# Performance work log

Measured on AMD Instinct MI355X. Metric: run time of the kernel, lower is better.

## Reference

```python
import jax, jax.numpy as jnp
import numpy as np

N, D, H, C = 50000, 256, 4, 16  # nodes, in_dim, heads, out_channels (hidden_dim)
E = 1600000
NEG_SLOPE = 0.2


def _gatv2_layer(x, src, dst, Wl, bl, Wr, br, att, bias, n_nodes):
    """PyG GATv2Conv (share_weights=False, concat=True, eval mode).
    x: [N, Fin]; Wl/Wr: [Fin, H*C]; att: [H, C]; bias: [H*C].
    """
    xl = (x @ Wl + bl).reshape(n_nodes, H, C)  # source-side transform
    xr = (x @ Wr + br).reshape(n_nodes, H, C)  # target-side transform
    # per-edge attention logits: a^T LeakyReLU(xl_j + xr_i)
    e = jax.nn.leaky_relu(xl[src] + xr[dst], negative_slope=NEG_SLOPE)  # [E,H,C]
    logits = jnp.einsum('ehc,hc->eh', e, att)  # [E,H]
    # scatter-softmax over incoming edges of each target node
    m = jax.ops.segment_max(logits, dst, num_segments=n_nodes)  # [N,H]
    ex = jnp.exp(logits - m[dst])
    denom = jax.ops.segment_sum(ex, dst, num_segments=n_nodes)  # [N,H]
    alpha = ex / denom[dst]  # [E,H]
    out = jax.ops.segment_sum(alpha[:, :, None] * xl[src], dst, num_segments=n_nodes)
    return out.reshape(n_nodes, H * C) + bias


def setup_inputs() -> dict:
    key = jax.random.key(0)
    ks = jax.random.split(key, 16)
    g = lambda k, shp, fan: jax.random.normal(k, shp, jnp.float32) * (1.0 / np.sqrt(fan))
    inp = {
        'x': jax.random.normal(ks[0], (N, D), jnp.float32),
        'edge_index': jax.random.randint(ks[1], (2, E), 0, N, dtype=jnp.int64),
        # conv1: in D -> H*C
        'Wl1': g(ks[2], (D, H * C), D), 'bl1': jnp.zeros((H * C,), jnp.float32),
        'Wr1': g(ks[3], (D, H * C), D), 'br1': jnp.zeros((H * C,), jnp.float32),
        'att1': g(ks[4], (H, C), C), 'bias1': jnp.zeros((H * C,), jnp.float32),
        # conv2: in H*C -> H*C
        'Wl2': g(ks[5], (H * C, H * C), H * C), 'bl2': jnp.zeros((H * C,), jnp.float32),
        'Wr2': g(ks[6], (H * C, H * C), H * C), 'br2': jnp.zeros((H * C,), jnp.float32),
        'att2': g(ks[7], (H, C), C), 'bias2': jnp.zeros((H * C,), jnp.float32),
        # output head: H*C -> D
        'Wo': g(ks[8], (H * C, D), H * C), 'bo': jnp.zeros((D,), jnp.float32),
    }
    return inp


def reference(x, edge_index, Wl1, bl1, Wr1, br1, att1, bias1,
              Wl2, bl2, Wr2, br2, att2, bias2, Wo, bo):
    src, dst = edge_index[0], edge_index[1]
    h = jax.nn.relu(_gatv2_layer(x, src, dst, Wl1, bl1, Wr1, br1, att1, bias1, N))
    h = jax.nn.relu(_gatv2_layer(h, src, dst, Wl2, bl2, Wr2, br2, att2, bias2, N))
    return jax.nn.sigmoid(h @ Wo + bo)  # min_max is None -> no affine rescale
```

## Files before the change

kernel.cpp:

```cpp
#include <hip/hip_runtime.h>
#include <math.h>

#define NN 50000
#define DIN 256
#define HC 64
#define NEG 0.2f
#define TM 64
#define NB 196
#define EPB 4096
#define CAP 36864

typedef short bf16x8 __attribute__((ext_vector_type(8)));
typedef unsigned short ush8 __attribute__((ext_vector_type(8)));
typedef float f32x4 __attribute__((ext_vector_type(4)));

__device__ __forceinline__ unsigned short f2bf(float x) {
    unsigned u = __float_as_uint(x);
    u += 0x7FFFu + ((u >> 16) & 1u);
    return (unsigned short)(u >> 16);
}
__device__ __forceinline__ float bf2f(unsigned short h) {
    return __uint_as_float((unsigned)h << 16);
}

template <int CTRL>
__device__ __forceinline__ float dpp_mov(float x) {
    int r = __builtin_amdgcn_update_dpp(0, __float_as_int(x), CTRL, 0xF, 0xF, true);
    return __int_as_float(r);
}


__global__ __launch_bounds__(256) void bhist_k(const int* __restrict__ dst,
                                               int* __restrict__ bcnt, int E) {
    __shared__ int h[NB];
    int t = threadIdx.x;
    for (int i = t; i < NB; i += 256) h[i] = 0;
    __syncthreads();
    int base = blockIdx.x * 2048 + t;
#pragma unroll
    for (int k = 0; k < 8; ++k) {
        int e = base + k * 256;
        if (e < E) atomicAdd(&h[dst[e] >> 8], 1);
    }
    __syncthreads();
    for (int i = t; i < NB; i += 256)
        if (h[i]) atomicAdd(&bcnt[i], h[i]);
}

__global__ __launch_bounds__(256) void bscan_k(const int* __restrict__ bcnt,
                                               int* __restrict__ boffs,
                                               int* __restrict__ bcursor,
                                               int* __restrict__ offs, int E) {
    __shared__ int s[256];
    int t = threadIdx.x;
    s[t] = (t < NB) ? bcnt[t] : 0;
    __syncthreads();
    for (int off = 1; off < 256; off <<= 1) {
        int v = s[t];
        int u = (t >= off) ? s[t - off] : 0;
        __syncthreads();
        s[t] = v + u;
        __syncthreads();
    }
    if (t < NB) {
        int ex = (t == 0) ? 0 : s[t - 1];
        boffs[t] = ex;
        bcursor[t] = ex;
    }
    if (t == NB) boffs[NB] = s[NB - 1];
    if (t == 0) offs[NN] = E;
}

__global__ __launch_bounds__(1024) void bin_k(const int* __restrict__ src,
                                              const int* __restrict__ dst,
                                              int* __restrict__ bcursor,
                                              unsigned* __restrict__ epair, int E) {
    __shared__ int hist[NB];
    __shared__ int lofs[NB];
    __shared__ int gshift[NB];
    __shared__ int scanb[256];
    __shared__ unsigned pbuf[EPB];
    __shared__ unsigned char abkt[EPB];
    int t = threadIdx.x;
    for (int i = t; i < NB; i += 1024) hist[i] = 0;
    __syncthreads();
    int e0 = blockIdx.x * EPB;
    unsigned p[4]; int bk[4], rk[4]; bool val[4];
#pragma unroll
    for (int k = 0; k < 4; ++k) {
        int e = e0 + k * 1024 + t;
        val[k] = e < E;
        if (val[k]) {
            int s = src[e], d = dst[e];
            p[k] = ((unsigned)s << 8) | (unsigned)(d & 255);
            bk[k] = d >> 8;
            rk[k] = atomicAdd(&hist[bk[k]], 1);
        }
    }
    __syncthreads();
    if (t < 256) scanb[t] = (t < NB) ? hist[t] : 0;
    __syncthreads();
    for (int off = 1; off < 256; off <<= 1) {
        int v = 0, u = 0;
        if (t < 256) { v = scanb[t]; if (t >= off) u = scanb[t - off]; }
        __syncthreads();
        if (t < 256) scanb[t] = v + u;
        __syncthreads();
    }
    if (t < NB) {
        int ex = (t == 0) ? 0 : scanb[t - 1];
        lofs[t] = ex;
        int gb = atomicAdd(&bcursor[t], hist[t]);
        gshift[t] = gb - ex;
    }
    __syncthreads();
    int total = scanb[NB - 1];
#pragma unroll
    for (int k = 0; k < 4; ++k) {
        if (val[k]) {
            int pos = lofs[bk[k]] + rk[k];
            pbuf[pos] = p[k];
            abkt[pos] = (unsigned char)bk[k];
        }
    }
    __syncthreads();
    for (int i = t; i < total; i += 1024) {
        int b = abkt[i];
        epair[gshift[b] + i] = pbuf[i];
    }
}

__global__ __launch_bounds__(1024) void bsort_k(const unsigned* __restrict__ epair,
                                                const int* __restrict__ boffs,
                                                int* __restrict__ offs,
                                                unsigned* __restrict__ ssrc, int n) {
    __shared__ int lhist[256];
    __shared__ int lcur[256];
    __shared__ int scanb[256];
    __shared__ unsigned sbuf[CAP];
    int b = blockIdx.x, t = threadIdx.x;
    int start = boffs[b], end = boffs[b + 1];
    int cnt = end - start;
    if (t < 256) lhist[t] = 0;
    __syncthreads();
    for (int i = t; i < cnt; i += 1024) {
        unsigned p = epair[start + i];
        atomicAdd(&lhist[p & 255], 1);
    }
    __syncthreads();
    if (t < 256) scanb[t] = lhist[t];
    __syncthreads();
    for (int off = 1; off < 256; off <<= 1) {
        int v = 0, u = 0;
        if (t < 256) { v = scanb[t]; if (t >= off) u = scanb[t - off]; }
        __syncthreads();
        if (t < 256) scanb[t] = v + u;
        __syncthreads();
    }
    if (t < 256) {
        int ex = (t == 0) ? 0 : scanb[t - 1];
        lcur[t] = ex;
        int node = b * 256 + t;
        if (node < n) offs[node] = start + ex;
    }
    __syncthreads();
    if (cnt <= CAP) {
        for (int i = t; i < cnt; i += 1024) {
            unsigned p = epair[start + i];
            int r = atomicAdd(&lcur[p & 255], 1);
            sbuf[r] = p & ~255u;
        }
        __syncthreads();
        for (int i = t; i < cnt; i += 1024) ssrc[start + i] = sbuf[i] >> 1;
    } else {
        for (int i = t; i < cnt; i += 1024) {
            unsigned p = epair[start + i];
            int r = atomicAdd(&lcur[p & 255], 1);
            ssrc[start + r] = (p & ~255u) >> 1;
        }
    }
}

__global__ __launch_bounds__(256) void wprep_dual_k(const float* __restrict__ Wl,
                                                    const float* __restrict__ Wr,
                                                    unsigned short* __restrict__ img,
                                                    int K) {
    int i = blockIdx.x * 256 + threadIdx.x;
    int total = (K >> 5) * 10240;
    if (i >= total) return;
    int kk = i % 40;
    int c  = (i / 40) & 127;
    int p  = (i / 5120) & 1;
    int s  = i / 10240;
    unsigned short v = 0;
    if (kk < 32) {
        int k = s * 32 + kk;
        float w = (c < 64) ? Wl[k * HC + c] : Wr[k * HC + (c - 64)];
        unsigned short hi = f2bf(w);
        v = p ? f2bf(w - bf2f(hi)) : hi;
    }
    img[i] = v;
}

__global__ __launch_bounds__(256) void wprep_head_k(const float* __restrict__ Wo,
                                                    unsigned short* __restrict__ img) {
    int i = blockIdx.x * 256 + threadIdx.x;
    if (i >= 40960) return;
    int kk = i % 40;
    int c  = (i / 40) & 127;
    int p  = (i / 5120) & 1;
    int s  = (i / 10240) & 1;
    int h  = i / 20480;
    unsigned short v = 0;
    if (kk < 32) {
        int k = s * 32 + kk;
        float w = Wo[k * DIN + h * 128 + c];
        unsigned short hi = f2bf(w);
        v = p ? f2bf(w - bf2f(hi)) : hi;
    }
    img[i] = v;
}

__global__ __launch_bounds__(256) void gemm_dual_mfma_k(
        const float* __restrict__ A,
        const unsigned short* __restrict__ img,
        const float* __restrict__ bl, const float* __restrict__ br,
        _Float16* __restrict__ xlh, float* __restrict__ xr,
        int n, int K) {
    __shared__ __attribute__((aligned(16))) unsigned short As[2][64][40];
    __shared__ __attribute__((aligned(16))) unsigned short Bs[2][128][40];
    int t = threadIdx.x;
    int l = t & 63, w = t >> 6;
    int wr = w >> 1, wc = w & 1;
    int lan = l & 15;
    int kb  = (l >> 4) * 8;
    int row0 = blockIdx.x * 64;
    int srow = t >> 2;
    int skq  = (t & 3) * 8;
    bool rok = (row0 + srow) < n;
    const float* aptr = A + (size_t)(row0 + srow) * K + skq;

    f32x4 acc0[4] = {}, acc1[4] = {};

    int nks = K >> 5;
    for (int ks = 0; ks < nks; ++ks) {
        __syncthreads();
        {
            const ush8* src = (const ush8*)(img + (size_t)ks * 10240);
            ush8* dst = (ush8*)&Bs[0][0][0];
            int base = w * 5 * 64 + l;
#pragma unroll
            for (int c2 = 0; c2 < 5; ++c2) {
                int u = base + c2 * 64;
                dst[u] = src[u];
            }
        }
        {
            float4 f0 = make_float4(0.f, 0.f, 0.f, 0.f), f1 = f0;
            if (rok) {
                f0 = *(const float4*)(aptr + ks * 32);
                f1 = *(const float4*)(aptr + ks * 32 + 4);
            }
            float xs[8] = {f0.x, f0.y, f0.z, f0.w, f1.x, f1.y, f1.z, f1.w};
            ush8 hi8, lo8;
#pragma unroll
            for (int j = 0; j < 8; ++j) {
                unsigned short h = f2bf(xs[j]);
                hi8[j] = h;
                lo8[j] = f2bf(xs[j] - bf2f(h));
            }
            *(ush8*)&As[0][srow][skq] = hi8;
            *(ush8*)&As[1][srow][skq] = lo8;
        }
        __syncthreads();
        bf16x8 ah0 = *(const bf16x8*)&As[0][wr * 32 + lan][kb];
        bf16x8 ah1 = *(const bf16x8*)&As[0][wr * 32 + 16 + lan][kb];
        bf16x8 al0 = *(const bf16x8*)&As[1][wr * 32 + lan][kb];
        bf16x8 al1 = *(const bf16x8*)&As[1][wr * 32 + 16 + lan][kb];
#pragma unroll
        for (int cf = 0; cf < 4; ++cf) {
            int bc = wc * 64 + cf * 16 + lan;
            bf16x8 bhv = *(const bf16x8*)&Bs[0][bc][kb];
            bf16x8 blv = *(const bf16x8*)&Bs[1][bc][kb];
            acc0[cf] = __builtin_amdgcn_mfma_f32_16x16x32_bf16(ah0, bhv, acc0[cf], 0, 0, 0);
            acc1[cf] = __builtin_amdgcn_mfma_f32_16x16x32_bf16(ah1, bhv, acc1[cf], 0, 0, 0);
            acc0[cf] = __builtin_amdgcn_mfma_f32_16x16x32_bf16(al0, bhv, acc0[cf], 0, 0, 0);
            acc1[cf] = __builtin_amdgcn_mfma_f32_16x16x32_bf16(al1, bhv, acc1[cf], 0, 0, 0);
            acc0[cf] = __builtin_amdgcn_mfma_f32_16x16x32_bf16(ah0, blv, acc0[cf], 0, 0, 0);
            acc1[cf] = __builtin_amdgcn_mfma_f32_16x16x32_bf16(ah1, blv, acc1[cf], 0, 0, 0);
        }
    }
#pragma unroll
    for (int cf = 0; cf < 4; ++cf) {
        int col = wc * 64 + cf * 16 + lan;
        bool left = col < 64;
        float bv = left ? bl[col] : br[col - 64];
        int c2 = left ? col : col - 64;
#pragma unroll
        for (int rf = 0; rf < 2; ++rf) {
            f32x4 a = rf ? acc1[cf] : acc0[cf];
            int rbase = row0 + wr * 32 + rf * 16 + (l >> 4) * 4;
#pragma unroll
            for (int r = 0; r < 4; ++r) {
                int grow = rbase + r;
                if (grow < n) {
                    float v = a[r] + bv;
                    if (left) xlh[(size_t)grow * HC + c2] = (_Float16)v;
                    else      xr[(size_t)grow * HC + c2] = v;
                }
            }
        }
    }
}

__global__ __launch_bounds__(256) void head_gemm_mfma_k(
        const float* __restrict__ A,
        const unsigned short* __restrict__ img,
        const float* __restrict__ bo,
        float* __restrict__ out, int n) {
    __shared__ __attribute__((aligned(16))) unsigned short As[2][64][40];
    __shared__ __attribute__((aligned(16))) unsigned short Bs[2][128][40];
    int t = threadIdx.x;
    int l = t & 63, w = t >> 6;
    int wr = w >> 1, wc = w & 1;
    int lan = l & 15;
    int kb  = (l >> 4) * 8;
    int row0 = blockIdx.x * 64;
    int coloff = blockIdx.y * 128;
    const unsigned short* himg = img + (size_t)blockIdx.y * 2 * 10240;
    int srow = t >> 2;
    int skq  = (t & 3) * 8;
    bool rok = (row0 + srow) < n;
    const float* aptr = A + (size_t)(row0 + srow) * HC + skq;

    f32x4 acc0[4] = {}, acc1[4] = {};

    for (int ks = 0; ks < 2; ++ks) {
        __syncthreads();
        {
            const ush8* src = (const ush8*)(himg + (size_t)ks * 10240);
            ush8* dst = (ush8*)&Bs[0][0][0];
            int base = w * 5 * 64 + l;
#pragma unroll
            for (int c2 = 0; c2 < 5; ++c2) {
                int u = base + c2 * 64;
                dst[u] = src[u];
            }
        }
        {
            float4 f0 = make_float4(0.f, 0.f, 0.f, 0.f), f1 = f0;
            if (rok) {
                f0 = *(const float4*)(aptr + ks * 32);
                f1 = *(const float4*)(aptr + ks * 32 + 4);
            }
            float xs[8] = {f0.x, f0.y, f0.z, f0.w, f1.x, f1.y, f1.z, f1.w};
            ush8 hi8, lo8;
#pragma unroll
            for (int j = 0; j < 8; ++j) {
                unsigned short h = f2bf(xs[j]);
                hi8[j] = h;
                lo8[j] = f2bf(xs[j] - bf2f(h));
            }
            *(ush8*)&As[0][srow][skq] = hi8;
            *(ush8*)&As[1][srow][skq] = lo8;
        }
        __syncthreads();
        bf16x8 ah0 = *(const bf16x8*)&As[0][wr * 32 + lan][kb];
        bf16x8 ah1 = *(const bf16x8*)&As[0][wr * 32 + 16 + lan][kb];
        bf16x8 al0 = *(const bf16x8*)&As[1][wr * 32 + lan][kb];
        bf16x8 al1 = *(const bf16x8*)&As[1][wr * 32 + 16 + lan][kb];
#pragma unroll
        for (int cf = 0; cf < 4; ++cf) {
            int bc = wc * 64 + cf * 16 + lan;
            bf16x8 bhv = *(const bf16x8*)&Bs[0][bc][kb];
            bf16x8 blv = *(const bf16x8*)&Bs[1][bc][kb];
            acc0[cf] = __builtin_amdgcn_mfma_f32_16x16x32_bf16(ah0, bhv, acc0[cf], 0, 0, 0);
            acc1[cf] = __builtin_amdgcn_mfma_f32_16x16x32_bf16(ah1, bhv, acc1[cf], 0, 0, 0);
            acc0[cf] = __builtin_amdgcn_mfma_f32_16x16x32_bf16(al0, bhv, acc0[cf], 0, 0, 0);
            acc1[cf] = __builtin_amdgcn_mfma_f32_16x16x32_bf16(al1, bhv, acc1[cf], 0, 0, 0);
            acc0[cf] = __builtin_amdgcn_mfma_f32_16x16x32_bf16(ah0, blv, acc0[cf], 0, 0, 0);
            acc1[cf] = __builtin_amdgcn_mfma_f32_16x16x32_bf16(ah1, blv, acc1[cf], 0, 0, 0);
        }
    }
#pragma unroll
    for (int cf = 0; cf < 4; ++cf) {
        int col = coloff + wc * 64 + cf * 16 + lan;
        float bv = bo[col];
#pragma unroll
        for (int rf = 0; rf < 2; ++rf) {
            f32x4 a = rf ? acc1[cf] : acc0[cf];
            int rbase = row0 + wr * 32 + rf * 16 + (l >> 4) * 4;
#pragma unroll
            for (int r = 0; r < 4; ++r) {
                int grow = rbase + r;
                if (grow < n) {
                    float v = a[r] + bv;
                    out[(size_t)grow * DIN + col] = 1.f / (1.f + __expf(-v));
                }
            }
        }
    }
}

union H4 { uint2 u; _Float16 h[4]; };

#define AGRP_BODY(SB)                                                         \
    {                                                                         \
        H4 cv;                                                                \
        cv.u = *(const uint2*)(xhb + (SB) + hoff);                            \
        float xv0 = (float)cv.h[0], xv1 = (float)cv.h[1];                     \
        float xv2 = (float)cv.h[2], xv3 = (float)cv.h[3];                     \
        float s0 = xv0 + xrq.x, s1 = xv1 + xrq.y;                             \
        float s2 = xv2 + xrq.z, s3 = xv3 + xrq.w;                             \
        float tt = atq.x * fmaxf(s0, NEG * s0);                               \
        tt = fmaf(atq.y, fmaxf(s1, NEG * s1), tt);                            \
        tt = fmaf(atq.z, fmaxf(s2, NEG * s2), tt);                            \
        tt = fmaf(atq.w, fmaxf(s3, NEG * s3), tt);                            \
        tt += dpp_mov<0xB1>(tt);                                              \
        tt += dpp_mov<0x4E>(tt);                                              \
        float ex = exp2f(tt);                                                 \
        den += ex;                                                            \
        acc.x = fmaf(ex, xv0, acc.x); acc.y = fmaf(ex, xv1, acc.y);           \
        acc.z = fmaf(ex, xv2, acc.z); acc.w = fmaf(ex, xv3, acc.w);           \
    }

#define AGRPS(KK)                                                             \
    {                                                                         \
        unsigned sb = (unsigned)__shfl((int)sbv, (KK) * 4 + q);               \
        AGRP_BODY(sb)                                                         \
    }

__global__ __launch_bounds__(256) void agg_k(const _Float16* __restrict__ xlh,
                                             const float* __restrict__ xr,
                                             const float* __restrict__ att,
                                             const float* __restrict__ bias,
                                             const int* __restrict__ offs,
                                             const unsigned* __restrict__ ssb,
                                             float* __restrict__ out, int n) {
    int wave = (blockIdx.x * 256 + threadIdx.x) >> 6;
    int lane = threadIdx.x & 63;
    if (wave >= n) return;
    int q  = lane >> 4;
    int sl = lane & 15;
    const char* xhb = (const char*)xlh;
    unsigned hoff = (unsigned)sl * 8u;
    float4 xrq = *(const float4*)(xr + (size_t)wave * HC + sl * 4);
    float4 atq = *(const float4*)(att + sl * 4);
    const float LOG2E = 1.44269504088896340736f;
    atq.x *= LOG2E; atq.y *= LOG2E; atq.z *= LOG2E; atq.w *= LOG2E;
    float4 acc = make_float4(0.f, 0.f, 0.f, 0.f);
    float den = 0.f;
    int lo = __builtin_amdgcn_readfirstlane(offs[wave]);
    int hi = __builtin_amdgcn_readfirstlane(offs[wave + 1]);
    int i = lo;
    for (; i + 32 <= hi; i += 32) {
        unsigned sbv = ssb[i + (lane & 31)];
        AGRPS(0) AGRPS(1) AGRPS(2) AGRPS(3)
        AGRPS(4) AGRPS(5) AGRPS(6) AGRPS(7)
    }
    for (; i + 16 <= hi; i += 16) {
        unsigned sbv = ssb[i + (lane & 15)];
        AGRPS(0) AGRPS(1) AGRPS(2) AGRPS(3)
    }
    for (; i < hi; i += 4) {
        int e = i + q;
        bool ok = e < hi;
        int ec = ok ? e : (hi - 1);
        unsigned sb = ssb[ec];
        H4 cv;
        cv.u = *(const uint2*)(xhb + sb + hoff);
        float xv0 = (float)cv.h[0], xv1 = (float)cv.h[1];
        float xv2 = (float)cv.h[2], xv3 = (float)cv.h[3];
        float s0 = xv0 + xrq.x, s1 = xv1 + xrq.y;
        float s2 = xv2 + xrq.z, s3 = xv3 + xrq.w;
        float tt = atq.x * fmaxf(s0, NEG * s0);
        tt = fmaf(atq.y, fmaxf(s1, NEG * s1), tt);
        tt = fmaf(atq.z, fmaxf(s2, NEG * s2), tt);
        tt = fmaf(atq.w, fmaxf(s3, NEG * s3), tt);
        tt += dpp_mov<0xB1>(tt);
        tt += dpp_mov<0x4E>(tt);
        float ex = exp2f(tt);
        ex = ok ? ex : 0.f;
        den += ex;
        acc.x = fmaf(ex, xv0, acc.x); acc.y = fmaf(ex, xv1, acc.y);
        acc.z = fmaf(ex, xv2, acc.z); acc.w = fmaf(ex, xv3, acc.w);
    }
#pragma unroll
    for (int m = 16; m < 64; m <<= 1) {
        acc.x += __shfl_xor(acc.x, m);
        acc.y += __shfl_xor(acc.y, m);
        acc.z += __shfl_xor(acc.z, m);
        acc.w += __shfl_xor(acc.w, m);
        den   += __shfl_xor(den, m);
    }
    if (q == 0) {
        float r = (den > 0.f) ? 1.f / den : 0.f;
        float4 b4 = *(const float4*)(bias + sl * 4);
        float4 o;
        o.x = fmaxf(fmaf(acc.x, r, b4.x), 0.f);
        o.y = fmaxf(fmaf(acc.y, r, b4.y), 0.f);
        o.z = fmaxf(fmaf(acc.z, r, b4.z), 0.f);
        o.w = fmaxf(fmaf(acc.w, r, b4.w), 0.f);
        *(float4*)(out + (size_t)wave * HC + sl * 4) = o;
    }
}

extern "C" void kernel_launch(void* const* d_in, const int* in_sizes, int n_in,
                              void* d_out, int out_size, void* d_ws, size_t ws_size,
                              hipStream_t stream) {
    const float* x    = (const float*)d_in[0];
    const int*   ei   = (const int*)d_in[1];
    const float* Wl1  = (const float*)d_in[2];
    const float* bl1  = (const float*)d_in[3];
    const float* Wr1  = (const float*)d_in[4];
    const float* br1  = (const float*)d_in[5];
    const float* att1 = (const float*)d_in[6];
    const float* bias1= (const float*)d_in[7];
    const float* Wl2  = (const float*)d_in[8];
    const float* bl2  = (const float*)d_in[9];
    const float* Wr2  = (const float*)d_in[10];
    const float* br2  = (const float*)d_in[11];
    const float* att2 = (const float*)d_in[12];
    const float* bias2= (const float*)d_in[13];
    const float* Wo   = (const float*)d_in[14];
    const float* bo   = (const float*)d_in[15];
    float* out = (float*)d_out;

    int E = in_sizes[1] / 2;
    const int* srcv = ei;
    const int* dstv = ei + E;

    size_t NF = (size_t)NN * HC;
    float* xl = (float*)d_ws;
    float* xr = xl + NF;
    float* hb = xr + NF;
    int* offs        = (int*)(hb + NF);
    unsigned* ssrc   = (unsigned*)(offs + NN + 1);
    int* boffs   = (int*)(ssrc + E);
    int* bcursor = boffs + NB + 1;
    int* bcnt    = bcursor + NB;
    unsigned* epair = (unsigned*)d_out;
    unsigned short* img1 = (unsigned short*)d_out;
    unsigned short* img2 = img1 + 81920;
    unsigned short* imgh = (unsigned short*)xl;
    _Float16* xlh = (_Float16*)((char*)d_out + (16u << 20));

    hipMemsetAsync(bcnt, 0, NB * sizeof(int), stream);
    bhist_k<<<(E + 2047) / 2048, 256, 0, stream>>>(dstv, bcnt, E);
    bscan_k<<<1, 256, 0, stream>>>(bcnt, boffs, bcursor, offs, E);
    bin_k<<<(E + EPB - 1) / EPB, 1024, 0, stream>>>(srcv, dstv, bcursor, epair, E);
    bsort_k<<<NB, 1024, 0, stream>>>(epair, boffs, offs, ssrc, NN);
    wprep_dual_k<<<320, 256, 0, stream>>>(Wl1, Wr1, img1, DIN);
    wprep_dual_k<<<80, 256, 0, stream>>>(Wl2, Wr2, img2, HC);

    int gb = (NN + TM - 1) / TM;
    gemm_dual_mfma_k<<<gb, 256, 0, stream>>>(x, img1, bl1, br1, xlh, xr, NN, DIN);
    agg_k<<<(NN + 3) / 4, 256, 0, stream>>>(xlh, xr, att1, bias1, offs, ssrc, hb, NN);
    gemm_dual_mfma_k<<<gb, 256, 0, stream>>>(hb, img2, bl2, br2, xlh, xr, NN, HC);
    agg_k<<<(NN + 3) / 4, 256, 0, stream>>>(xlh, xr, att2, bias2, offs, ssrc, hb, NN);
    wprep_head_k<<<160, 256, 0, stream>>>(Wo, imgh);
    head_gemm_mfma_k<<<dim3(gb, 2), 256, 0, stream>>>(hb, imgh, bo, out, NN);
}
```

Before: 319.7 us.

## Widen aggregation lanes to 8 halves per lane, 8 edges per wave step

The per-node aggregation kernel now gives each lane 8 fp16 features (a 16-byte load) instead of 4, so a wave handles 8 edges at a time instead of 4. The head-sum reduction needs one DPP step instead of two, and the main loop consumes 64 edges per iteration. Tail handling is split into 32/16/8 blocks plus a masked remainder. This raises per-lane register use and leaves more lanes idle on nodes with few edges, in exchange for fewer gather instructions and fewer cross-lane reductions per edge.

Measured after the change: 345.3 us. 8.0% more time.

```diff
diff --git a/kernel.cpp b/kernel.cpp
--- a/kernel.cpp
+++ b/kernel.cpp
@@ -402,32 +402,42 @@
     }
 }
 
-union H4 { uint2 u; _Float16 h[4]; };
-
-#define AGRP_BODY(SB)                                                         \
+union H8 { uint4 u; _Float16 s[8]; };
+
+#define AGRP8(SB, OK)                                                         \
     {                                                                         \
-        H4 cv;                                                                \
-        cv.u = *(const uint2*)(xhb + (SB) + hoff);                            \
-        float xv0 = (float)cv.h[0], xv1 = (float)cv.h[1];                     \
-        float xv2 = (float)cv.h[2], xv3 = (float)cv.h[3];                     \
-        float s0 = xv0 + xrq.x, s1 = xv1 + xrq.y;                             \
-        float s2 = xv2 + xrq.z, s3 = xv3 + xrq.w;                             \
-        float tt = atq.x * fmaxf(s0, NEG * s0);                               \
-        tt = fmaf(atq.y, fmaxf(s1, NEG * s1), tt);                            \
-        tt = fmaf(atq.z, fmaxf(s2, NEG * s2), tt);                            \
-        tt = fmaf(atq.w, fmaxf(s3, NEG * s3), tt);                            \
-        tt += dpp_mov<0xB1>(tt);                                              \
-        tt += dpp_mov<0x4E>(tt);                                              \
+        H8 cv;                                                                \
+        cv.u = *(const uint4*)(xhb + (SB) + hoff);                            \
+        float xv0 = (float)cv.s[0], xv1 = (float)cv.s[1];                     \
+        float xv2 = (float)cv.s[2], xv3 = (float)cv.s[3];                     \
+        float xv4 = (float)cv.s[4], xv5 = (float)cv.s[5];                     \
+        float xv6 = (float)cv.s[6], xv7 = (float)cv.s[7];                     \
+        float s0 = xv0 + xr0, s1 = xv1 + xr1;                                 \
+        float s2 = xv2 + xr2, s3 = xv3 + xr3;                                 \
+        float s4 = xv4 + xr4, s5 = xv5 + xr5;                                 \
+        float s6 = xv6 + xr6, s7 = xv7 + xr7;                                 \
+        float tt = at0 * fmaxf(s0, NEG * s0);                                 \
+        tt = fmaf(at1, fmaxf(s1, NEG * s1), tt);                              \
+        tt = fmaf(at2, fmaxf(s2, NEG * s2), tt);                              \
+        tt = fmaf(at3, fmaxf(s3, NEG * s3), tt);                              \
+        tt = fmaf(at4, fmaxf(s4, NEG * s4), tt);                              \
+        tt = fmaf(at5, fmaxf(s5, NEG * s5), tt);                              \
+        tt = fmaf(at6, fmaxf(s6, NEG * s6), tt);                              \
+        tt = fmaf(at7, fmaxf(s7, NEG * s7), tt);                              \
+        tt += dpp_mov<0xB1>(tt);       \
         float ex = exp2f(tt);                                                 \
+        if (!(OK)) ex = 0.f;                                                  \
         den += ex;                                                            \
-        acc.x = fmaf(ex, xv0, acc.x); acc.y = fmaf(ex, xv1, acc.y);           \
-        acc.z = fmaf(ex, xv2, acc.z); acc.w = fmaf(ex, xv3, acc.w);           \
-    }
-
-#define AGRPS(KK)                                                             \
+        a0 = fmaf(ex, xv0, a0); a1 = fmaf(ex, xv1, a1);                       \
+        a2 = fmaf(ex, xv2, a2); a3 = fmaf(ex, xv3, a3);                       \
+        a4 = fmaf(ex, xv4, a4); a5 = fmaf(ex, xv5, a5);                       \
+        a6 = fmaf(ex, xv6, a6); a7 = fmaf(ex, xv7, a7);                       \
+    }
+
+#define AGRPS8(KK)                                                            \
     {                                                                         \
-        unsigned sb = (unsigned)__shfl((int)sbv, (KK) * 4 + q);               \
-        AGRP_BODY(sb)                                                         \
+        unsigned sb = (unsigned)__shfl((int)sbv, (KK) * 8 + q);               \
+        AGRP8(sb, true)                                                       \
     }
 
 __global__ __launch_bounds__(256) void agg_k(const _Float16* __restrict__ xlh,
@@ -440,68 +450,81 @@
     int wave = (blockIdx.x * 256 + threadIdx.x) >> 6;
     int lane = threadIdx.x & 63;
     if (wave >= n) return;
-    int q  = lane >> 4;
-    int sl = lane & 15;
+    int q  = lane >> 3;
+    int sl = lane & 7;
     const char* xhb = (const char*)xlh;
-    unsigned hoff = (unsigned)sl * 8u;
-    float4 xrq = *(const float4*)(xr + (size_t)wave * HC + sl * 4);
-    float4 atq = *(const float4*)(att + sl * 4);
+    unsigned hoff = (unsigned)sl * 16u;
+    const float* xp = xr + (size_t)wave * HC + sl * 8;
+    float4 xq0 = *(const float4*)xp;
+    float4 xq1 = *(const float4*)(xp + 4);
+    float xr0 = xq0.x, xr1 = xq0.y, xr2 = xq0.z, xr3 = xq0.w;
+    float xr4 = xq1.x, xr5 = xq1.y, xr6 = xq1.z, xr7 = xq1.w;
     const float LOG2E = 1.44269504088896340736f;
-    atq.x *= LOG2E; atq.y *= LOG2E; atq.z *= LOG2E; atq.w *= LOG2E;
-    float4 acc = make_float4(0.f, 0.f, 0.f, 0.f);
+    const float* ap = att + sl * 8;
+    float4 aq0 = *(const float4*)ap;
+    float4 aq1 = *(const float4*)(ap + 4);
+    float at0 = aq0.x * LOG2E, at1 = aq0.y * LOG2E;
+    float at2 = aq0.z * LOG2E, at3 = aq0.w * LOG2E;
+    float at4 = aq1.x * LOG2E, at5 = aq1.y * LOG2E;
+    float at6 = aq1.z * LOG2E, at7 = aq1.w * LOG2E;
+
+    float a0 = 0.f, a1 = 0.f, a2 = 0.f, a3 = 0.f;
+    float a4 = 0.f, a5 = 0.f, a6 = 0.f, a7 = 0.f;
     float den = 0.f;
     int lo = __builtin_amdgcn_readfirstlane(offs[wave]);
     int hi = __builtin_amdgcn_readfirstlane(offs[wave + 1]);
     int i = lo;
-    for (; i + 32 <= hi; i += 32) {
+    for (; i + 64 <= hi; i += 64) {
+        unsigned sbv = ssb[i + lane];
+        AGRPS8(0) AGRPS8(1) AGRPS8(2) AGRPS8(3)
+        AGRPS8(4) AGRPS8(5) AGRPS8(6) AGRPS8(7)
+    }
+    if (i + 32 <= hi) {
         unsigned sbv = ssb[i + (lane & 31)];
-        AGRPS(0) AGRPS(1) AGRPS(2) AGRPS(3)
-        AGRPS(4) AGRPS(5) AGRPS(6) AGRPS(7)
-    }
-    for (; i + 16 <= hi; i += 16) {
+        AGRPS8(0) AGRPS8(1) AGRPS8(2) AGRPS8(3)
+        i += 32;
+    }
+    if (i + 16 <= hi) {
         unsigned sbv = ssb[i + (lane & 15)];
-        AGRPS(0) AGRPS(1) AGRPS(2) AGRPS(3)
-    }
-    for (; i < hi; i += 4) {
+        AGRPS8(0) AGRPS8(1)
+        i += 16;
+    }
+    if (i + 8 <= hi) {
+        unsigned sbv = ssb[i + (lane & 7)];
+        AGRPS8(0)
+        i += 8;
+    }
+    for (; i < hi; i += 8) {
         int e = i + q;
         bool ok = e < hi;
-        int ec = ok ? e : (hi - 1);
-        unsigned sb = ssb[ec];
-        H4 cv;
-        cv.u = *(const uint2*)(xhb + sb + hoff);
-        float xv0 = (float)cv.h[0], xv1 = (float)cv.h[1];
-        float xv2 = (float)cv.h[2], xv3 = (float)cv.h[3];
-        float s0 = xv0 + xrq.x, s1 = xv1 + xrq.y;
-        float s2 = xv2 + xrq.z, s3 = xv3 + xrq.w;
-        float tt = atq.x * fmaxf(s0, NEG * s0);
-        tt = fmaf(atq.y, fmaxf(s1, NEG * s1), tt);
-        tt = fmaf(atq.z, fmaxf(s2, NEG * s2), tt);
-        tt = fmaf(atq.w, fmaxf(s3, NEG * s3), tt);
-        tt += dpp_mov<0xB1>(tt);
-        tt += dpp_mov<0x4E>(tt);
-        float ex = exp2f(tt);
-        ex = ok ? ex : 0.f;
-        den += ex;
-        acc.x = fmaf(ex, xv0, acc.x); acc.y = fmaf(ex, xv1, acc.y);
-        acc.z = fmaf(ex, xv2, acc.z); acc.w = fmaf(ex, xv3, acc.w);
-    }
-#pragma unroll
-    for (int m = 16; m < 64; m <<= 1) {
-        acc.x += __shfl_xor(acc.x, m);
-        acc.y += __shfl_xor(acc.y, m);
-        acc.z += __shfl_xor(acc.z, m);
-        acc.w += __shfl_xor(acc.w, m);
-        den   += __shfl_xor(den, m);
+        unsigned sb = ssb[ok ? e : (hi - 1)];
+        AGRP8(sb, ok)
+    }
+#pragma unroll
+    for (int m = 8; m < 64; m <<= 1) {
+        a0 += __shfl_xor(a0, m); a1 += __shfl_xor(a1, m);
+        a2 += __shfl_xor(a2, m); a3 += __shfl_xor(a3, m);
+        a4 += __shfl_xor(a4, m); a5 += __shfl_xor(a5, m);
+        a6 += __shfl_xor(a6, m); a7 += __shfl_xor(a7, m);
+        den += __shfl_xor(den, m);
     }
     if (q == 0) {
         float r = (den > 0.f) ? 1.f / den : 0.f;
-        float4 b4 = *(const float4*)(bias + sl * 4);
-        float4 o;
-        o.x = fmaxf(fmaf(acc.x, r, b4.x), 0.f);
-        o.y = fmaxf(fmaf(acc.y, r, b4.y), 0.f);
-        o.z = fmaxf(fmaf(acc.z, r, b4.z), 0.f);
-        o.w = fmaxf(fmaf(acc.w, r, b4.w), 0.f);
-        *(float4*)(out + (size_t)wave * HC + sl * 4) = o;
+        const float* bp = bias + sl * 8;
+        float4 b0 = *(const float4*)bp;
+        float4 b1 = *(const float4*)(bp + 4);
+        float4 o0, o1;
+        o0.x = fmaxf(fmaf(a0, r, b0.x), 0.f);
+        o0.y = fmaxf(fmaf(a1, r, b0.y), 0.f);
+        o0.z = fmaxf(fmaf(a2, r, b0.z), 0.f);
+        o0.w = fmaxf(fmaf(a3, r, b0.w), 0.f);
+        o1.x = fmaxf(fmaf(a4, r, b1.x), 0.f);
+        o1.y = fmaxf(fmaf(a5, r, b1.y), 0.f);
+        o1.z = fmaxf(fmaf(a6, r, b1.z), 0.f);
+        o1.w = fmaxf(fmaf(a7, r, b1.w), 0.f);
+        float* op = out + (size_t)wave * HC + sl * 8;
+        *(float4*)op = o0;
+        *(float4*)(op + 4) = o1;
     }
 }
 
```
